# Kernel tuning notes

Measured on AMD Instinct MI355X. Metric: run time of the kernel, lower is better.

The kernel has to match this reference:

```python
import jax, jax.numpy as jnp
import numpy as np

N = 30000       # nodes
E = 480000      # edges (before self loops)
IN = 128        # in_channels
H1, C1 = 5, 64  # conv1 heads, per-head channels
OUT = 64        # out_channels (conv2, heads=1)
PE = 100000     # pos/neg edges for decode
NEG_SLOPE = 0.2


def setup_inputs() -> dict:
    key = jax.random.key(0)
    ks = jax.random.split(key, 12)
    return {
        "x": jax.random.normal(ks[0], (N, IN), dtype=jnp.float32),
        "edge_index": jax.random.randint(ks[1], (2, E), 0, N),
        "pos_edge_index": jax.random.randint(ks[2], (2, PE), 0, N),
        "neg_edge_index": jax.random.randint(ks[3], (2, PE), 0, N),
        "W1": jax.random.normal(ks[4], (IN, H1 * C1), dtype=jnp.float32) * 0.05,
        "att_src1": jax.random.normal(ks[5], (H1, C1), dtype=jnp.float32) * 0.1,
        "att_dst1": jax.random.normal(ks[6], (H1, C1), dtype=jnp.float32) * 0.1,
        "b1": jnp.zeros((H1 * C1,), dtype=jnp.float32),
        "W2": jax.random.normal(ks[7], (H1 * C1, OUT), dtype=jnp.float32) * 0.05,
        "att_src2": jax.random.normal(ks[8], (1, OUT), dtype=jnp.float32) * 0.1,
        "att_dst2": jax.random.normal(ks[9], (1, OUT), dtype=jnp.float32) * 0.1,
        "b2": jnp.zeros((OUT,), dtype=jnp.float32),
    }


def gat_conv(x, edge_index, W, att_src, att_dst, bias, heads, out_ch):
    """PyG GATConv: add self loops, linear proj, edge softmax, scatter-sum, concat heads."""
    n = x.shape[0]
    loops = jnp.arange(n)
    src = jnp.concatenate([edge_index[0], loops])  # message sources j
    dst = jnp.concatenate([edge_index[1], loops])  # message targets i
    h = (x @ W).reshape(n, heads, out_ch)          # [N,H,C]
    a_src = jnp.sum(h * att_src, axis=-1)          # [N,H]
    a_dst = jnp.sum(h * att_dst, axis=-1)          # [N,H]
    e = jax.nn.leaky_relu(a_src[src] + a_dst[dst], NEG_SLOPE)  # [E',H]
    # numerically-stable segment softmax over incoming edges of each dst node
    m = jax.ops.segment_max(e, dst, num_segments=n)
    m = jax.lax.stop_gradient(jnp.where(jnp.isfinite(m), m, 0.0))
    ex = jnp.exp(e - m[dst])
    s = jax.ops.segment_sum(ex, dst, num_segments=n)
    alpha = ex / (s[dst] + 1e-16)                  # [E',H]
    out = jax.ops.segment_sum(alpha[:, :, None] * h[src], dst, num_segments=n)  # [N,H,C]
    return out.reshape(n, heads * out_ch) + bias


def reference(x, edge_index, pos_edge_index, neg_edge_index,
              W1, att_src1, att_dst1, b1, W2, att_src2, att_dst2, b2):
    z = gat_conv(x, edge_index, W1, att_src1, att_dst1, b1, H1, C1)
    z = jax.nn.relu(z)
    z = gat_conv(z, edge_index, W2, att_src2, att_dst2, b2, 1, OUT)
    ei = jnp.concatenate([pos_edge_index, neg_edge_index], axis=-1)
    return jnp.sum(z[ei[0]] * z[ei[1]], axis=-1)  # [2*PE]
```

## Files before the change

### kernel.cpp

```cpp
#include <hip/hip_runtime.h>
#include <hip/hip_fp16.h>
#include <cstdint>
#include <cstddef>
#include <type_traits>

#define N_NODES 30000
#define N_EDGES 480000
#define N_EDGES_SL (N_EDGES + N_NODES)
#define IN_CH 128
#define HEADS1 5
#define C1 64
#define D1 (HEADS1 * C1)
#define OUT_CH 64
#define PE_CNT 100000
#define NEG_SLOPE 0.2f
#define BCAP 64
#define GEMM1_BLOCKS 469
#define BUCKET_BLOCKS 128

typedef _Float16 f16x8 __attribute__((ext_vector_type(8)));
typedef _Float16 f16x2 __attribute__((ext_vector_type(2)));
typedef float fx4 __attribute__((ext_vector_type(4)));

#if defined(__has_builtin)
#if __has_builtin(__builtin_amdgcn_fdot2)
#define HAS_FDOT2 1
#endif
#endif

static __device__ __forceinline__ float leaky(float x) {
    return x > 0.f ? x : NEG_SLOPE * x;
}

template<int NH, typename AT>
static __device__ __forceinline__ void gemm_phase(const AT* __restrict__ A,
                                                  const __half* __restrict__ Wt,
                                                  __half* __restrict__ C, int K,
                                                  const float* __restrict__ att_src,
                                                  const float* __restrict__ att_dst,
                                                  float* __restrict__ as_out,
                                                  float* __restrict__ ad_out,
                                                  int slot, int nsl, int lane) {
    const int N = NH * 64;
    int q = lane >> 4, l16 = lane & 15;
    for (int tile = slot; tile < N_NODES / 16; tile += nsl) {
        int rowBase = tile * 16;
        int arow = rowBase + l16;
        fx4 zero4 = {0.f, 0.f, 0.f, 0.f};
        fx4 acc[NH][4];
#pragma unroll
        for (int h = 0; h < NH; ++h)
#pragma unroll
            for (int c = 0; c < 4; ++c) acc[h][c] = zero4;
        for (int kk = 0; kk < K; kk += 32) {
            f16x8 af;
            if constexpr (std::is_same<AT, float>::value) {
                const float4* s = (const float4*)(A + (size_t)arow * K + kk + q * 8);
                float4 v0 = s[0], v1 = s[1];
                af[0] = (_Float16)v0.x; af[1] = (_Float16)v0.y;
                af[2] = (_Float16)v0.z; af[3] = (_Float16)v0.w;
                af[4] = (_Float16)v1.x; af[5] = (_Float16)v1.y;
                af[6] = (_Float16)v1.z; af[7] = (_Float16)v1.w;
            } else {
                af = *(const f16x8*)((const __half*)A + (size_t)arow * K + kk + q * 8);
            }
#pragma unroll
            for (int h = 0; h < NH; ++h) {
#pragma unroll
                for (int c = 0; c < 4; ++c) {
                    int col = h * 64 + c * 16 + l16;
                    f16x8 bf = *(const f16x8*)(Wt + (size_t)col * K + kk + q * 8);
                    acc[h][c] = __builtin_amdgcn_mfma_f32_16x16x32_f16(af, bf, acc[h][c], 0, 0, 0);
                }
            }
        }
#pragma unroll
        for (int h = 0; h < NH; ++h) {
            float ps[4] = {0.f, 0.f, 0.f, 0.f};
            float pd[4] = {0.f, 0.f, 0.f, 0.f};
#pragma unroll
            for (int c = 0; c < 4; ++c) {
                int gcol = h * 64 + c * 16 + l16;
                float av = att_src[gcol];
                float dv = att_dst[gcol];
#pragma unroll
                for (int reg = 0; reg < 4; ++reg) {
                    int grow = rowBase + q * 4 + reg;
                    float val = acc[h][c][reg];
                    C[(size_t)grow * N + gcol] = __float2half(val);
                    ps[reg] += val * av;
                    pd[reg] += val * dv;
                }
            }
#pragma unroll
            for (int off = 1; off < 16; off <<= 1) {
#pragma unroll
                for (int reg = 0; reg < 4; ++reg) {
                    ps[reg] += __shfl_xor(ps[reg], off, 64);
                    pd[reg] += __shfl_xor(pd[reg], off, 64);
                }
            }
            if (l16 == 0) {
#pragma unroll
                for (int reg = 0; reg < 4; ++reg) {
                    int grow = rowBase + q * 4 + reg;
                    as_out[(size_t)h * N_NODES + grow] = ps[reg];
                    ad_out[(size_t)h * N_NODES + grow] = pd[reg];
                }
            }
        }
    }
}

__global__ __launch_bounds__(256) void k_init(int* __restrict__ cnt,
                                              const float* __restrict__ W1,
                                              __half* __restrict__ Wt1,
                                              const float* __restrict__ W2,
                                              __half* __restrict__ Wt2) {
    int t = blockIdx.x * 256 + threadIdx.x;
    int nthr = gridDim.x * 256;
    for (int i = t; i < N_NODES + 8; i += nthr) cnt[i] = 0;
    const int T1 = IN_CH * D1, T2 = D1 * OUT_CH;
    for (int idx = t; idx < T1 + T2; idx += nthr) {
        if (idx < T1) {
            int k = idx / D1, n = idx - k * D1;
            Wt1[(size_t)n * IN_CH + k] = __float2half(W1[idx]);
        } else {
            int i2 = idx - T1;
            int k = i2 / OUT_CH, n = i2 - k * OUT_CH;
            Wt2[(size_t)n * D1 + k] = __float2half(W2[i2]);
        }
    }
}

__global__ __launch_bounds__(256) void k_build_gemm1(const int* __restrict__ edge,
                                                     int* __restrict__ cnt,
                                                     int* __restrict__ esrc2,
                                                     int* __restrict__ ovf_cnt,
                                                     int* __restrict__ ovf,
                                                     const float* __restrict__ x,
                                                     const __half* __restrict__ Wt1,
                                                     __half* __restrict__ h1,
                                                     const float* __restrict__ att_src1,
                                                     const float* __restrict__ att_dst1,
                                                     float* __restrict__ as1,
                                                     float* __restrict__ ad1) {
    int lane = threadIdx.x & 63, wv = threadIdx.x >> 6;
    if (blockIdx.x < GEMM1_BLOCKS) {
        gemm_phase<HEADS1, float>(x, Wt1, h1, IN_CH, att_src1, att_dst1, as1, ad1,
                                  blockIdx.x * 4 + wv, GEMM1_BLOCKS * 4, lane);
    } else {
        int t = (blockIdx.x - GEMM1_BLOCKS) * 256 + threadIdx.x;
        int nthr = BUCKET_BLOCKS * 256;
        for (int e = t; e < N_EDGES_SL; e += nthr) {
            int s, d;
            if (e < N_EDGES) { s = edge[e]; d = edge[N_EDGES + e]; }
            else { s = e - N_EDGES; d = s; }
            int r = atomicAdd(&cnt[d], 1);
            if (r < BCAP) {
                esrc2[d * BCAP + r] = s;
            } else {
                int oi = atomicAdd(ovf_cnt, 1);
                ovf[2 * oi] = d;
                ovf[2 * oi + 1] = s;
            }
        }
    }
}

template<int NH, bool RELU>
__global__ __launch_bounds__(256) void k_attn_agg(const int* __restrict__ cnt,
                                                  const int* __restrict__ esrc2,
                                                  const int* __restrict__ ovf_cnt,
                                                  const int* __restrict__ ovf,
                                                  const __half* __restrict__ hf,
                                                  const float* __restrict__ a_src,
                                                  const float* __restrict__ a_dst,
                                                  const float* __restrict__ bias,
                                                  __half* __restrict__ zout) {
    __shared__ unsigned wpk[4][64];
    __shared__ int jbuf[4][64];
    __shared__ float red[4][584];
    int wid = (blockIdx.x * 256 + threadIdx.x) >> 6;
    int lane = threadIdx.x & 63;
    int wv = threadIdx.x >> 6;
    if (wid >= N_NODES * NH) return;
    int h = wid / N_NODES;
    int node = wid - h * N_NODES;
    int deg = cnt[node];
    const float* asrc_h = a_src + (size_t)h * N_NODES;
    float adst = a_dst[(size_t)h * N_NODES + node];
    const int RS = NH * 64;
    if (deg <= BCAP) {
        int es = lane >> 3, cg = lane & 7;
        const __half* hbase = hf + h * 64 + cg * 8;
        int j = 0;
        float ex = 0.f;
        if (lane < deg) {
            j = esrc2[node * BCAP + lane];
            ex = __expf(leaky(asrc_h[j] + adst));
        }
        float s = ex;
#pragma unroll
        for (int off = 1; off < 64; off <<= 1)
            s += __shfl_xor(s, off, 64);
        float r = 1.f / (s + 1e-16f);
        __half2 wn = __float2half2_rn(ex * r);
        wpk[wv][lane] = *(unsigned*)&wn;
        jbuf[wv][lane] = j;
        __half2 acch[4] = {__half2{0, 0}, __half2{0, 0}, __half2{0, 0}, __half2{0, 0}};
        for (int k0 = 0; k0 < deg; k0 += 32) {
            int kA = k0 + es, kB = k0 + 8 + es, kC = k0 + 16 + es, kD = k0 + 24 + es;
            bool oA = kA < deg, oB = kB < deg, oC = kC < deg, oD = kD < deg;
            unsigned uA = oA ? wpk[wv][kA] : 0u;
            unsigned uB = oB ? wpk[wv][kB] : 0u;
            unsigned uC = oC ? wpk[wv][kC] : 0u;
            unsigned uD = oD ? wpk[wv][kD] : 0u;
            int jA = jbuf[wv][oA ? kA : 0];
            int jB = jbuf[wv][oB ? kB : 0];
            int jC = jbuf[wv][oC ? kC : 0];
            int jD = jbuf[wv][oD ? kD : 0];
            float4 vA = *(const float4*)(hbase + (size_t)jA * RS);
            float4 vB = *(const float4*)(hbase + (size_t)jB * RS);
            float4 vC = *(const float4*)(hbase + (size_t)jC * RS);
            float4 vD = *(const float4*)(hbase + (size_t)jD * RS);
            __half2 hwA = *(__half2*)&uA, hwB = *(__half2*)&uB;
            __half2 hwC = *(__half2*)&uC, hwD = *(__half2*)&uD;
            const __half2* pA = (const __half2*)&vA;
            const __half2* pB = (const __half2*)&vB;
            const __half2* pC = (const __half2*)&vC;
            const __half2* pD = (const __half2*)&vD;
#pragma unroll
            for (int i = 0; i < 4; ++i) {
                acch[i] = __hfma2(pA[i], hwA, acch[i]);
                acch[i] = __hfma2(pB[i], hwB, acch[i]);
                acch[i] = __hfma2(pC[i], hwC, acch[i]);
                acch[i] = __hfma2(pD[i], hwD, acch[i]);
            }
        }
#pragma unroll
        for (int i = 0; i < 4; ++i) {
            float2 f = __half22float2(acch[i]);
            red[wv][(cg * 8 + 2 * i) * 9 + es] = f.x;
            red[wv][(cg * 8 + 2 * i + 1) * 9 + es] = f.y;
        }
        float tot = 0.f;
#pragma unroll
        for (int e2 = 0; e2 < 8; ++e2)
            tot += red[wv][lane * 9 + e2];
        float o = tot + bias[h * 64 + lane];
        if (RELU) o = fmaxf(o, 0.f);
        zout[(size_t)node * RS + h * 64 + lane] = __float2half(o);
    } else {
        int ovn = *ovf_cnt;
        int jb = esrc2[node * BCAP + lane];
        float s = __expf(leaky(asrc_h[jb] + adst));
#pragma unroll
        for (int off = 1; off < 64; off <<= 1)
            s += __shfl_xor(s, off, 64);
        float s2 = 0.f;
        for (int k = lane; k < ovn; k += 64)
            if (ovf[2 * k] == node)
                s2 += __expf(leaky(asrc_h[ovf[2 * k + 1]] + adst));
#pragma unroll
        for (int off = 1; off < 64; off <<= 1)
            s2 += __shfl_xor(s2, off, 64);
        float r = 1.f / (s + s2 + 1e-16f);
        float a = 0.f;
        for (int k = 0; k < BCAP; ++k) {
            int j = esrc2[node * BCAP + k];
            float w = __expf(leaky(asrc_h[j] + adst));
            a += w * __half2float(hf[(size_t)j * RS + h * 64 + lane]);
        }
        for (int k = 0; k < ovn; ++k) {
            if (ovf[2 * k] == node) {
                int j = ovf[2 * k + 1];
                float w = __expf(leaky(asrc_h[j] + adst));
                a += w * __half2float(hf[(size_t)j * RS + h * 64 + lane]);
            }
        }
        float o = a * r + bias[h * 64 + lane];
        if (RELU) o = fmaxf(o, 0.f);
        zout[(size_t)node * RS + h * 64 + lane] = __float2half(o);
    }
}

__global__ __launch_bounds__(256) void k_gemm2(const __half* __restrict__ z1,
                                               const __half* __restrict__ Wt2,
                                               __half* __restrict__ h2,
                                               const float* __restrict__ att_src2,
                                               const float* __restrict__ att_dst2,
                                               float* __restrict__ as2,
                                               float* __restrict__ ad2) {
    int lane = threadIdx.x & 63, wv = threadIdx.x >> 6;
    gemm_phase<1, __half>(z1, Wt2, h2, D1, att_src2, att_dst2, as2, ad2,
                          blockIdx.x * 4 + wv, gridDim.x * 4, lane);
}

__global__ __launch_bounds__(256) void k_decode(const int* __restrict__ pos,
                                                const int* __restrict__ neg,
                                                const __half* __restrict__ z2,
                                                float* __restrict__ out) {
    int t = blockIdx.x * 256 + threadIdx.x;
    int e = t >> 3;
    int lc = t & 7;
    if (e >= 2 * PE_CNT) return;
    int a, b;
    if (e < PE_CNT) { a = pos[e]; b = pos[PE_CNT + e]; }
    else { int k = e - PE_CNT; a = neg[k]; b = neg[PE_CNT + k]; }
    union U { float4 f; f16x2 h[4]; __half2 hh[4]; } ua, ub;
    ua.f = *(const float4*)(z2 + (size_t)a * OUT_CH + lc * 8);
    ub.f = *(const float4*)(z2 + (size_t)b * OUT_CH + lc * 8);
    float v = 0.f;
#pragma unroll
    for (int i = 0; i < 4; ++i) {
#ifdef HAS_FDOT2
        v = __builtin_amdgcn_fdot2(ua.h[i], ub.h[i], v, false);
#else
        float2 fa = __half22float2(ua.hh[i]);
        float2 fb = __half22float2(ub.hh[i]);
        v += fa.x * fb.x + fa.y * fb.y;
#endif
    }
#pragma unroll
    for (int off = 1; off < 8; off <<= 1)
        v += __shfl_xor(v, off, 64);
    if (lc == 0) out[e] = v;
}

extern "C" void kernel_launch(void* const* d_in, const int* in_sizes, int n_in,
                              void* d_out, int out_size, void* d_ws, size_t ws_size,
                              hipStream_t stream) {
    const float* x        = (const float*)d_in[0];
    const int* edge_index = (const int*)d_in[1];
    const int* pos_ei     = (const int*)d_in[2];
    const int* neg_ei     = (const int*)d_in[3];
    const float* W1       = (const float*)d_in[4];
    const float* att_src1 = (const float*)d_in[5];
    const float* att_dst1 = (const float*)d_in[6];
    const float* b1       = (const float*)d_in[7];
    const float* W2       = (const float*)d_in[8];
    const float* att_src2 = (const float*)d_in[9];
    const float* att_dst2 = (const float*)d_in[10];
    const float* b2       = (const float*)d_in[11];
    float* out            = (float*)d_out;

    char* ws = (char*)d_ws;
    size_t off = 0;
    auto alloc = [&](size_t bytes) -> void* {
        void* p = ws + off;
        off = (off + bytes + 255) & ~(size_t)255;
        return p;
    };
    int* cnt     = (int*)alloc(sizeof(int) * (N_NODES + 8));
    int* ovfc    = cnt + N_NODES;
    int* esrc2   = (int*)alloc(sizeof(int) * (size_t)N_NODES * BCAP);
    int* ovf     = (int*)alloc(sizeof(int) * (size_t)2 * N_EDGES_SL);
    __half* h1   = (__half*)alloc(sizeof(__half) * (size_t)N_NODES * D1);
    __half* z1   = (__half*)alloc(sizeof(__half) * (size_t)N_NODES * D1);
    __half* h2   = (__half*)alloc(sizeof(__half) * (size_t)N_NODES * OUT_CH);
    __half* z2   = (__half*)alloc(sizeof(__half) * (size_t)N_NODES * OUT_CH);
    __half* Wt1  = (__half*)alloc(sizeof(__half) * (size_t)D1 * IN_CH);
    __half* Wt2  = (__half*)alloc(sizeof(__half) * (size_t)OUT_CH * D1);
    float* as1   = (float*)alloc(sizeof(float) * (size_t)N_NODES * HEADS1);
    float* ad1   = (float*)alloc(sizeof(float) * (size_t)N_NODES * HEADS1);
    float* as2   = (float*)alloc(sizeof(float) * (size_t)N_NODES);
    float* ad2   = (float*)alloc(sizeof(float) * (size_t)N_NODES);

    k_init<<<240, 256, 0, stream>>>(cnt, W1, Wt1, W2, Wt2);
    k_build_gemm1<<<GEMM1_BLOCKS + BUCKET_BLOCKS, 256, 0, stream>>>(
        edge_index, cnt, esrc2, ovfc, ovf, x, Wt1, h1, att_src1, att_dst1, as1, ad1);
    k_attn_agg<HEADS1, true><<<(N_NODES * HEADS1 + 3) / 4, 256, 0, stream>>>(
        cnt, esrc2, ovfc, ovf, h1, as1, ad1, b1, z1);
    k_gemm2<<<469, 256, 0, stream>>>(z1, Wt2, h2, att_src2, att_dst2, as2, ad2);
    k_attn_agg<1, false><<<(N_NODES + 3) / 4, 256, 0, stream>>>(
        cnt, esrc2, ovfc, ovf, h2, as2, ad2, b2, z2);
    k_decode<<<(2 * PE_CNT * 8 + 255) / 256, 256, 0, stream>>>(pos_ei, neg_ei, z2, out);

    (void)in_sizes; (void)n_in; (void)out_size; (void)ws_size;
}
```

Baseline: 213.2 us.

## Fuse layer-1 attention aggregation with layer-2 GEMM via shared-memory node tiles

Layer-1 aggregation now processes all five heads per node inside one wave and stages a 16-node tile of ReLU'd z1 rows in shared memory. The same block then runs an MFMA GEMM against Wt2 and computes the layer-2 attention scores, replacing the separate gemm2 kernel. This removes the z1 global write and re-read and one launch, and it shares the edge-list load and softmax setup across heads. The cost is fewer waves in flight, since there is one block per 16 nodes and each wave loops over 4 nodes and 5 heads serially, plus extra barriers.

New measurement: 219.8 us. +3.1%, slower.

```diff
diff --git a/kernel.cpp b/kernel.cpp
--- a/kernel.cpp
+++ b/kernel.cpp
@@ -168,37 +168,201 @@
     }
 }
 
-template<int NH, bool RELU>
-__global__ __launch_bounds__(256) void k_attn_agg(const int* __restrict__ cnt,
-                                                  const int* __restrict__ esrc2,
-                                                  const int* __restrict__ ovf_cnt,
-                                                  const int* __restrict__ ovf,
-                                                  const __half* __restrict__ hf,
-                                                  const float* __restrict__ a_src,
-                                                  const float* __restrict__ a_dst,
-                                                  const float* __restrict__ bias,
-                                                  __half* __restrict__ zout) {
+__global__ __launch_bounds__(256) void k_agg1g2(
+    const int* __restrict__ cnt, const int* __restrict__ esrc2,
+    const int* __restrict__ ovf_cnt, const int* __restrict__ ovf,
+    const __half* __restrict__ h1,
+    const float* __restrict__ as1, const float* __restrict__ ad1,
+    const float* __restrict__ b1,
+    const __half* __restrict__ Wt2,
+    const float* __restrict__ att_s2, const float* __restrict__ att_d2,
+    __half* __restrict__ h2, float* __restrict__ as2, float* __restrict__ ad2) {
+    __shared__ unsigned wpk[4][HEADS1][64];
+    __shared__ int jbuf[4][64];
+    __shared__ float red[4][584];
+    __shared__ __align__(16) __half zrow[16][D1];
+    __shared__ float spart[4][16], dpart[4][16];
+    int lane = threadIdx.x & 63, wv = threadIdx.x >> 6;
+    int q = lane >> 4, l16 = lane & 15;
+    int es = lane >> 3, cg = lane & 7;
+    int nodeBase = blockIdx.x * 16;
+
+    for (int i = 0; i < 4; ++i) {
+        int node = nodeBase + wv * 4 + i;
+        int zr = wv * 4 + i;
+        int deg = cnt[node];
+        if (deg <= BCAP) {
+            int j = 0;
+            if (lane < deg) j = esrc2[node * BCAP + lane];
+            jbuf[wv][lane] = j;
+            float ex[HEADS1], s[HEADS1];
+#pragma unroll
+            for (int h = 0; h < HEADS1; ++h) {
+                ex[h] = (lane < deg)
+                    ? __expf(leaky(as1[(size_t)h * N_NODES + j] + ad1[(size_t)h * N_NODES + node]))
+                    : 0.f;
+                s[h] = ex[h];
+            }
+#pragma unroll
+            for (int off = 1; off < 64; off <<= 1)
+#pragma unroll
+                for (int h = 0; h < HEADS1; ++h)
+                    s[h] += __shfl_xor(s[h], off, 64);
+#pragma unroll
+            for (int h = 0; h < HEADS1; ++h) {
+                float r = 1.f / (s[h] + 1e-16f);
+                __half2 wn = __float2half2_rn(ex[h] * r);
+                wpk[wv][h][lane] = *(unsigned*)&wn;
+            }
+#pragma unroll
+            for (int h = 0; h < HEADS1; ++h) {
+                const __half* hbase = h1 + h * 64 + cg * 8;
+                __half2 acch[4] = {__half2{0, 0}, __half2{0, 0}, __half2{0, 0}, __half2{0, 0}};
+                for (int k0 = 0; k0 < deg; k0 += 32) {
+                    int kA = k0 + es, kB = k0 + 8 + es, kC = k0 + 16 + es, kD = k0 + 24 + es;
+                    bool oA = kA < deg, oB = kB < deg, oC = kC < deg, oD = kD < deg;
+                    unsigned uA = oA ? wpk[wv][h][kA] : 0u;
+                    unsigned uB = oB ? wpk[wv][h][kB] : 0u;
+                    unsigned uC = oC ? wpk[wv][h][kC] : 0u;
+                    unsigned uD = oD ? wpk[wv][h][kD] : 0u;
+                    int jA = jbuf[wv][oA ? kA : 0];
+                    int jB = jbuf[wv][oB ? kB : 0];
+                    int jC = jbuf[wv][oC ? kC : 0];
+                    int jD = jbuf[wv][oD ? kD : 0];
+                    float4 vA = *(const float4*)(hbase + (size_t)jA * D1);
+                    float4 vB = *(const float4*)(hbase + (size_t)jB * D1);
+                    float4 vC = *(const float4*)(hbase + (size_t)jC * D1);
+                    float4 vD = *(const float4*)(hbase + (size_t)jD * D1);
+                    __half2 hwA = *(__half2*)&uA, hwB = *(__half2*)&uB;
+                    __half2 hwC = *(__half2*)&uC, hwD = *(__half2*)&uD;
+                    const __half2* pA = (const __half2*)&vA;
+                    const __half2* pB = (const __half2*)&vB;
+                    const __half2* pC = (const __half2*)&vC;
+                    const __half2* pD = (const __half2*)&vD;
+#pragma unroll
+                    for (int t2 = 0; t2 < 4; ++t2) {
+                        acch[t2] = __hfma2(pA[t2], hwA, acch[t2]);
+                        acch[t2] = __hfma2(pB[t2], hwB, acch[t2]);
+                        acch[t2] = __hfma2(pC[t2], hwC, acch[t2]);
+                        acch[t2] = __hfma2(pD[t2], hwD, acch[t2]);
+                    }
+                }
+#pragma unroll
+                for (int t2 = 0; t2 < 4; ++t2) {
+                    float2 f = __half22float2(acch[t2]);
+                    red[wv][(cg * 8 + 2 * t2) * 9 + es] = f.x;
+                    red[wv][(cg * 8 + 2 * t2 + 1) * 9 + es] = f.y;
+                }
+                float tot = 0.f;
+#pragma unroll
+                for (int e2 = 0; e2 < 8; ++e2)
+                    tot += red[wv][lane * 9 + e2];
+                float o = fmaxf(tot + b1[h * 64 + lane], 0.f);
+                zrow[zr][h * 64 + lane] = __float2half(o);
+            }
+        } else {
+            int ovn = *ovf_cnt;
+#pragma unroll
+            for (int h = 0; h < HEADS1; ++h) {
+                const float* asrc_h = as1 + (size_t)h * N_NODES;
+                float adst = ad1[(size_t)h * N_NODES + node];
+                float sl = __expf(leaky(asrc_h[esrc2[node * BCAP + lane]] + adst));
+#pragma unroll
+                for (int off = 1; off < 64; off <<= 1)
+                    sl += __shfl_xor(sl, off, 64);
+                float s2 = 0.f;
+                for (int k = lane; k < ovn; k += 64)
+                    if (ovf[2 * k] == node)
+                        s2 += __expf(leaky(asrc_h[ovf[2 * k + 1]] + adst));
+#pragma unroll
+                for (int off = 1; off < 64; off <<= 1)
+                    s2 += __shfl_xor(s2, off, 64);
+                float r = 1.f / (sl + s2 + 1e-16f);
+                float a = 0.f;
+                for (int k = 0; k < BCAP; ++k) {
+                    int jj = esrc2[node * BCAP + k];
+                    float w = __expf(leaky(asrc_h[jj] + adst));
+                    a += w * __half2float(h1[(size_t)jj * D1 + h * 64 + lane]);
+                }
+                for (int k = 0; k < ovn; ++k) {
+                    if (ovf[2 * k] == node) {
+                        int jj = ovf[2 * k + 1];
+                        float w = __expf(leaky(asrc_h[jj] + adst));
+                        a += w * __half2float(h1[(size_t)jj * D1 + h * 64 + lane]);
+                    }
+                }
+                float o = fmaxf(a * r + b1[h * 64 + lane], 0.f);
+                zrow[zr][h * 64 + lane] = __float2half(o);
+            }
+        }
+    }
+    __syncthreads();
+    fx4 acc = {0.f, 0.f, 0.f, 0.f};
+    int col = wv * 16 + l16;
+    for (int kk = 0; kk < D1; kk += 32) {
+        f16x8 af = *(const f16x8*)&zrow[l16][kk + q * 8];
+        f16x8 bf = *(const f16x8*)(Wt2 + (size_t)col * D1 + kk + q * 8);
+        acc = __builtin_amdgcn_mfma_f32_16x16x32_f16(af, bf, acc, 0, 0, 0);
+    }
+    float ps[4], pd[4];
+    {
+        float av = att_s2[col], dv = att_d2[col];
+#pragma unroll
+        for (int reg = 0; reg < 4; ++reg) {
+            int row = q * 4 + reg;
+            float val = acc[reg];
+            h2[(size_t)(nodeBase + row) * OUT_CH + col] = __float2half(val);
+            ps[reg] = val * av;
+            pd[reg] = val * dv;
+        }
+    }
+#pragma unroll
+    for (int off = 1; off < 16; off <<= 1)
+#pragma unroll
+        for (int reg = 0; reg < 4; ++reg) {
+            ps[reg] += __shfl_xor(ps[reg], off, 64);
+            pd[reg] += __shfl_xor(pd[reg], off, 64);
+        }
+    if (l16 == 0) {
+#pragma unroll
+        for (int reg = 0; reg < 4; ++reg) {
+            spart[wv][q * 4 + reg] = ps[reg];
+            dpart[wv][q * 4 + reg] = pd[reg];
+        }
+    }
+    __syncthreads();
+    if (wv == 0 && lane < 16) {
+        as2[nodeBase + lane] = spart[0][lane] + spart[1][lane] + spart[2][lane] + spart[3][lane];
+        ad2[nodeBase + lane] = dpart[0][lane] + dpart[1][lane] + dpart[2][lane] + dpart[3][lane];
+    }
+}
+
+__global__ __launch_bounds__(256) void k_attn_agg2(const int* __restrict__ cnt,
+                                                   const int* __restrict__ esrc2,
+                                                   const int* __restrict__ ovf_cnt,
+                                                   const int* __restrict__ ovf,
+                                                   const __half* __restrict__ hf,
+                                                   const float* __restrict__ a_src,
+                                                   const float* __restrict__ a_dst,
+                                                   const float* __restrict__ bias,
+                                                   __half* __restrict__ zout) {
     __shared__ unsigned wpk[4][64];
     __shared__ int jbuf[4][64];
     __shared__ float red[4][584];
-    int wid = (blockIdx.x * 256 + threadIdx.x) >> 6;
+    int node = (blockIdx.x * 256 + threadIdx.x) >> 6;
     int lane = threadIdx.x & 63;
     int wv = threadIdx.x >> 6;
-    if (wid >= N_NODES * NH) return;
-    int h = wid / N_NODES;
-    int node = wid - h * N_NODES;
+    if (node >= N_NODES) return;
     int deg = cnt[node];
-    const float* asrc_h = a_src + (size_t)h * N_NODES;
-    float adst = a_dst[(size_t)h * N_NODES + node];
-    const int RS = NH * 64;
+    float adst = a_dst[node];
     if (deg <= BCAP) {
         int es = lane >> 3, cg = lane & 7;
-        const __half* hbase = hf + h * 64 + cg * 8;
+        const __half* hbase = hf + cg * 8;
         int j = 0;
         float ex = 0.f;
         if (lane < deg) {
             j = esrc2[node * BCAP + lane];
-            ex = __expf(leaky(asrc_h[j] + adst));
+            ex = __expf(leaky(a_src[j] + adst));
         }
         float s = ex;
 #pragma unroll
@@ -220,10 +384,10 @@
             int jB = jbuf[wv][oB ? kB : 0];
             int jC = jbuf[wv][oC ? kC : 0];
             int jD = jbuf[wv][oD ? kD : 0];
-            float4 vA = *(const float4*)(hbase + (size_t)jA * RS);
-            float4 vB = *(const float4*)(hbase + (size_t)jB * RS);
-            float4 vC = *(const float4*)(hbase + (size_t)jC * RS);
-            float4 vD = *(const float4*)(hbase + (size_t)jD * RS);
+            float4 vA = *(const float4*)(hbase + (size_t)jA * OUT_CH);
+            float4 vB = *(const float4*)(hbase + (size_t)jB * OUT_CH);
+            float4 vC = *(const float4*)(hbase + (size_t)jC * OUT_CH);
+            float4 vD = *(const float4*)(hbase + (size_t)jD * OUT_CH);
             __half2 hwA = *(__half2*)&uA, hwB = *(__half2*)&uB;
             __half2 hwC = *(__half2*)&uC, hwD = *(__half2*)&uD;
             const __half2* pA = (const __half2*)&vA;
@@ -231,37 +395,34 @@
             const __half2* pC = (const __half2*)&vC;
             const __half2* pD = (const __half2*)&vD;
 #pragma unroll
-            for (int i = 0; i < 4; ++i) {
-                acch[i] = __hfma2(pA[i], hwA, acch[i]);
-                acch[i] = __hfma2(pB[i], hwB, acch[i]);
-                acch[i] = __hfma2(pC[i], hwC, acch[i]);
-                acch[i] = __hfma2(pD[i], hwD, acch[i]);
-            }
-        }
-#pragma unroll
-        for (int i = 0; i < 4; ++i) {
-            float2 f = __half22float2(acch[i]);
-            red[wv][(cg * 8 + 2 * i) * 9 + es] = f.x;
-            red[wv][(cg * 8 + 2 * i + 1) * 9 + es] = f.y;
+            for (int t2 = 0; t2 < 4; ++t2) {
+                acch[t2] = __hfma2(pA[t2], hwA, acch[t2]);
+                acch[t2] = __hfma2(pB[t2], hwB, acch[t2]);
+                acch[t2] = __hfma2(pC[t2], hwC, acch[t2]);
+                acch[t2] = __hfma2(pD[t2], hwD, acch[t2]);
+            }
+        }
+#pragma unroll
+        for (int t2 = 0; t2 < 4; ++t2) {
+            float2 f = __half22float2(acch[t2]);
+            red[wv][(cg * 8 + 2 * t2) * 9 + es] = f.x;
+            red[wv][(cg * 8 + 2 * t2 + 1) * 9 + es] = f.y;
         }
         float tot = 0.f;
 #pragma unroll
         for (int e2 = 0; e2 < 8; ++e2)
             tot += red[wv][lane * 9 + e2];
-        float o = tot + bias[h * 64 + lane];
-        if (RELU) o = fmaxf(o, 0.f);
-        zout[(size_t)node * RS + h * 64 + lane] = __float2half(o);
+        zout[(size_t)node * OUT_CH + lane] = __float2half(tot + bias[lane]);
     } else {
         int ovn = *ovf_cnt;
-        int jb = esrc2[node * BCAP + lane];
-        float s = __expf(leaky(asrc_h[jb] + adst));
+        float s = __expf(leaky(a_src[esrc2[node * BCAP + lane]] + adst));
 #pragma unroll
         for (int off = 1; off < 64; off <<= 1)
             s += __shfl_xor(s, off, 64);
         float s2 = 0.f;
         for (int k = lane; k < ovn; k += 64)
             if (ovf[2 * k] == node)
-                s2 += __expf(leaky(asrc_h[ovf[2 * k + 1]] + adst));
+                s2 += __expf(leaky(a_src[ovf[2 * k + 1]] + adst));
 #pragma unroll
         for (int off = 1; off < 64; off <<= 1)
             s2 += __shfl_xor(s2, off, 64);
@@ -269,32 +430,18 @@
         float a = 0.f;
         for (int k = 0; k < BCAP; ++k) {
             int j = esrc2[node * BCAP + k];
-            float w = __expf(leaky(asrc_h[j] + adst));
-            a += w * __half2float(hf[(size_t)j * RS + h * 64 + lane]);
+            float w = __expf(leaky(a_src[j] + adst));
+            a += w * __half2float(hf[(size_t)j * OUT_CH + lane]);
         }
         for (int k = 0; k < ovn; ++k) {
             if (ovf[2 * k] == node) {
                 int j = ovf[2 * k + 1];
-                float w = __expf(leaky(asrc_h[j] + adst));
-                a += w * __half2float(hf[(size_t)j * RS + h * 64 + lane]);
-            }
-        }
-        float o = a * r + bias[h * 64 + lane];
-        if (RELU) o = fmaxf(o, 0.f);
-        zout[(size_t)node * RS + h * 64 + lane] = __float2half(o);
-    }
-}
-
-__global__ __launch_bounds__(256) void k_gemm2(const __half* __restrict__ z1,
-                                               const __half* __restrict__ Wt2,
-                                               __half* __restrict__ h2,
-                                               const float* __restrict__ att_src2,
-                                               const float* __restrict__ att_dst2,
-                                               float* __restrict__ as2,
-                                               float* __restrict__ ad2) {
-    int lane = threadIdx.x & 63, wv = threadIdx.x >> 6;
-    gemm_phase<1, __half>(z1, Wt2, h2, D1, att_src2, att_dst2, as2, ad2,
-                          blockIdx.x * 4 + wv, gridDim.x * 4, lane);
+                float w = __expf(leaky(a_src[j] + adst));
+                a += w * __half2float(hf[(size_t)j * OUT_CH + lane]);
+            }
+        }
+        zout[(size_t)node * OUT_CH + lane] = __float2half(a * r + bias[lane]);
+    }
 }
 
 __global__ __launch_bounds__(256) void k_decode(const int* __restrict__ pos,
@@ -357,7 +504,6 @@
     int* esrc2   = (int*)alloc(sizeof(int) * (size_t)N_NODES * BCAP);
     int* ovf     = (int*)alloc(sizeof(int) * (size_t)2 * N_EDGES_SL);
     __half* h1   = (__half*)alloc(sizeof(__half) * (size_t)N_NODES * D1);
-    __half* z1   = (__half*)alloc(sizeof(__half) * (size_t)N_NODES * D1);
     __half* h2   = (__half*)alloc(sizeof(__half) * (size_t)N_NODES * OUT_CH);
     __half* z2   = (__half*)alloc(sizeof(__half) * (size_t)N_NODES * OUT_CH);
     __half* Wt1  = (__half*)alloc(sizeof(__half) * (size_t)D1 * IN_CH);
@@ -370,10 +516,10 @@
     k_init<<<240, 256, 0, stream>>>(cnt, W1, Wt1, W2, Wt2);
     k_build_gemm1<<<GEMM1_BLOCKS + BUCKET_BLOCKS, 256, 0, stream>>>(
         edge_index, cnt, esrc2, ovfc, ovf, x, Wt1, h1, att_src1, att_dst1, as1, ad1);
-    k_attn_agg<HEADS1, true><<<(N_NODES * HEADS1 + 3) / 4, 256, 0, stream>>>(
-        cnt, esrc2, ovfc, ovf, h1, as1, ad1, b1, z1);
-    k_gemm2<<<469, 256, 0, stream>>>(z1, Wt2, h2, att_src2, att_dst2, as2, ad2);
-    k_attn_agg<1, false><<<(N_NODES + 3) / 4, 256, 0, stream>>>(
+    k_agg1g2<<<N_NODES / 16, 256, 0, stream>>>(
+        cnt, esrc2, ovfc, ovf, h1, as1, ad1, b1, Wt2, att_src2, att_dst2,
+        h2, as2, ad2);
+    k_attn_agg2<<<(N_NODES + 3) / 4, 256, 0, stream>>>(
         cnt, esrc2, ovfc, ovf, h2, as2, ad2, b2, z2);
     k_decode<<<(2 * PE_CNT * 8 + 255) / 256, 256, 0, stream>>>(pos_ei, neg_ei, z2, out);
 
```

## Compute attention weights inline with deferred normalization, drop LDS staging

Applied to the files above, without the earlier changes.

The aggregation kernel no longer stages per-edge weights and source indices in shared memory. Instead each lane group reads neighbor indices straight from the bucket, computes unnormalized exp weights inline, accumulates in fp32, and applies the softmax normalization once after reduction. This removes the first wave-wide reduction pass and the LDS round trip, and fp32 accumulation replaces half2 FMAs. In exchange each edge's exp is recomputed redundantly by 8 lanes, the unroll drops from 4 to 2 gathers per iteration, and there is more VALU work per element.

Measured after the change: 214.9 us. No clear change (+0.8%).

```diff
diff --git a/kernel.cpp b/kernel.cpp
--- a/kernel.cpp
+++ b/kernel.cpp
@@ -178,8 +178,6 @@
                                                   const float* __restrict__ a_dst,
                                                   const float* __restrict__ bias,
                                                   __half* __restrict__ zout) {
-    __shared__ unsigned wpk[4][64];
-    __shared__ int jbuf[4][64];
     __shared__ float red[4][584];
     int wid = (blockIdx.x * 256 + threadIdx.x) >> 6;
     int lane = threadIdx.x & 63;
@@ -194,67 +192,48 @@
     if (deg <= BCAP) {
         int es = lane >> 3, cg = lane & 7;
         const __half* hbase = hf + h * 64 + cg * 8;
-        int j = 0;
-        float ex = 0.f;
-        if (lane < deg) {
-            j = esrc2[node * BCAP + lane];
-            ex = __expf(leaky(asrc_h[j] + adst));
-        }
-        float s = ex;
-#pragma unroll
-        for (int off = 1; off < 64; off <<= 1)
-            s += __shfl_xor(s, off, 64);
-        float r = 1.f / (s + 1e-16f);
-        __half2 wn = __float2half2_rn(ex * r);
-        wpk[wv][lane] = *(unsigned*)&wn;
-        jbuf[wv][lane] = j;
-        __half2 acch[4] = {__half2{0, 0}, __half2{0, 0}, __half2{0, 0}, __half2{0, 0}};
-        for (int k0 = 0; k0 < deg; k0 += 32) {
-            int kA = k0 + es, kB = k0 + 8 + es, kC = k0 + 16 + es, kD = k0 + 24 + es;
-            bool oA = kA < deg, oB = kB < deg, oC = kC < deg, oD = kD < deg;
-            unsigned uA = oA ? wpk[wv][kA] : 0u;
-            unsigned uB = oB ? wpk[wv][kB] : 0u;
-            unsigned uC = oC ? wpk[wv][kC] : 0u;
-            unsigned uD = oD ? wpk[wv][kD] : 0u;
-            int jA = jbuf[wv][oA ? kA : 0];
-            int jB = jbuf[wv][oB ? kB : 0];
-            int jC = jbuf[wv][oC ? kC : 0];
-            int jD = jbuf[wv][oD ? kD : 0];
+        const int* bkt = esrc2 + node * BCAP;
+        float acc[8] = {};
+        float ssum = 0.f;
+        for (int k0 = 0; k0 < deg; k0 += 16) {
+            int kA = k0 + es, kB = k0 + 8 + es;
+            bool oA = kA < deg, oB = kB < deg;
+            int jA = bkt[oA ? kA : 0];
+            int jB = bkt[oB ? kB : 0];
+            float eA = asrc_h[jA];
+            float eB = asrc_h[jB];
             float4 vA = *(const float4*)(hbase + (size_t)jA * RS);
             float4 vB = *(const float4*)(hbase + (size_t)jB * RS);
-            float4 vC = *(const float4*)(hbase + (size_t)jC * RS);
-            float4 vD = *(const float4*)(hbase + (size_t)jD * RS);
-            __half2 hwA = *(__half2*)&uA, hwB = *(__half2*)&uB;
-            __half2 hwC = *(__half2*)&uC, hwD = *(__half2*)&uD;
+            float wA = oA ? __expf(leaky(eA + adst)) : 0.f;
+            float wB = oB ? __expf(leaky(eB + adst)) : 0.f;
+            ssum += wA + wB;
             const __half2* pA = (const __half2*)&vA;
             const __half2* pB = (const __half2*)&vB;
-            const __half2* pC = (const __half2*)&vC;
-            const __half2* pD = (const __half2*)&vD;
 #pragma unroll
             for (int i = 0; i < 4; ++i) {
-                acch[i] = __hfma2(pA[i], hwA, acch[i]);
-                acch[i] = __hfma2(pB[i], hwB, acch[i]);
-                acch[i] = __hfma2(pC[i], hwC, acch[i]);
-                acch[i] = __hfma2(pD[i], hwD, acch[i]);
-            }
-        }
-#pragma unroll
-        for (int i = 0; i < 4; ++i) {
-            float2 f = __half22float2(acch[i]);
-            red[wv][(cg * 8 + 2 * i) * 9 + es] = f.x;
-            red[wv][(cg * 8 + 2 * i + 1) * 9 + es] = f.y;
-        }
+                float2 fA = __half22float2(pA[i]);
+                float2 fB = __half22float2(pB[i]);
+                acc[2 * i]     += wA * fA.x + wB * fB.x;
+                acc[2 * i + 1] += wA * fA.y + wB * fB.y;
+            }
+        }
+#pragma unroll
+        for (int m = 8; m < 64; m <<= 1)
+            ssum += __shfl_xor(ssum, m, 64);
+        float r = 1.f / (ssum + 1e-16f);
+#pragma unroll
+        for (int i = 0; i < 8; ++i)
+            red[wv][(cg * 8 + i) * 9 + es] = acc[i];
         float tot = 0.f;
 #pragma unroll
         for (int e2 = 0; e2 < 8; ++e2)
             tot += red[wv][lane * 9 + e2];
-        float o = tot + bias[h * 64 + lane];
+        float o = tot * r + bias[h * 64 + lane];
         if (RELU) o = fmaxf(o, 0.f);
         zout[(size_t)node * RS + h * 64 + lane] = __float2half(o);
     } else {
         int ovn = *ovf_cnt;
-        int jb = esrc2[node * BCAP + lane];
-        float s = __expf(leaky(asrc_h[jb] + adst));
+        float s = __expf(leaky(asrc_h[esrc2[node * BCAP + lane]] + adst));
 #pragma unroll
         for (int off = 1; off < 64; off <<= 1)
             s += __shfl_xor(s, off, 64);
```
